# Kernel optimization log

Hardware: AMD Instinct MI355X
Metric: run time of the kernel (lower is better)

Reference implementation:

```python
import jax, jax.numpy as jnp
import numpy as np

N, E, G = 50000, 600000, 512
F_IN, H, OUT = 128, 128, 256


def setup_inputs() -> dict:
    key = jax.random.key(0)
    ks = jax.random.split(key, 16)
    x = jax.random.normal(ks[0], (N, F_IN), dtype=jnp.float32)
    edge_index = jax.random.randint(ks[1], (2, E), 0, N, dtype=jnp.int64)
    batch = jnp.sort(jax.random.randint(ks[2], (N,), 0, G, dtype=jnp.int64))
    def lin(k, out_d, in_d):
        s = 1.0 / np.sqrt(in_d)
        return jax.random.uniform(k, (out_d, in_d), jnp.float32, -s, s)
    W1l, W1r = lin(ks[3], H, F_IN), lin(ks[4], H, F_IN)
    b1 = jnp.zeros((H,), jnp.float32)
    W2l, W2r = lin(ks[5], H, H), lin(ks[6], H, H)
    b2 = jnp.zeros((H,), jnp.float32)
    W3l, W3r = lin(ks[7], H, H), lin(ks[8], H, H)
    b3 = jnp.zeros((H,), jnp.float32)
    Wlin = lin(ks[9], OUT, 2 * H)
    blin = jnp.zeros((OUT,), jnp.float32)
    return dict(x=x, edge_index=edge_index, batch=batch,
                W1l=W1l, b1=b1, W1r=W1r, W2l=W2l, b2=b2, W2r=W2r,
                W3l=W3l, b3=b3, W3r=W3r, Wlin=Wlin, blin=blin)


def reference(x, edge_index, batch, W1l, b1, W1r, W2l, b2, W2r, W3l, b3, W3r, Wlin, blin):
    src, dst = edge_index[0], edge_index[1]
    # in-degree of each target node (mean aggregation denominator)
    deg = jax.ops.segment_sum(jnp.ones((E,), x.dtype), dst, num_segments=N)
    deg = jnp.maximum(deg, 1.0)[:, None]

    def sage(h, Wl, bl, Wr):
        # mean-aggregate neighbor features then linear; plus root transform
        agg = jax.ops.segment_sum(h[src], dst, num_segments=N) / deg
        return agg @ Wl.T + bl + h @ Wr.T

    h = jax.nn.relu(sage(x, W1l, b1, W1r))
    h = jax.nn.relu(sage(h, W2l, b2, W2r))
    h = sage(h, W3l, b3, W3r)

    # global max / mean pool per graph
    x_max = jax.ops.segment_max(h, batch, num_segments=G)
    x_max = jnp.where(jnp.isfinite(x_max), x_max, 0.0)
    cnt = jnp.maximum(jax.ops.segment_sum(jnp.ones((N,), h.dtype), batch, num_segments=G), 1.0)
    x_mean = jax.ops.segment_sum(h, batch, num_segments=G) / cnt[:, None]

    pooled = jnp.concatenate([x_max, x_mean], axis=1)  # [G, 2H]
    # dropout is identity in eval mode
    return pooled @ Wlin.T + blin
```

## Files before the change

### kernel.cpp

```cpp
#include <hip/hip_runtime.h>
#include <hip/hip_bf16.h>
#include <hip/hip_fp16.h>


#define FH 128
#define OUTD 256
#define SLOTS 64
#define PWB 96

typedef unsigned int u32;
typedef unsigned short u16;
typedef __attribute__((ext_vector_type(8))) _Float16 f16frag;
typedef __attribute__((ext_vector_type(4))) float f4frag;

typedef __attribute__((address_space(3))) u32 lds_u32;
typedef __attribute__((address_space(1))) const u32 glb_u32;

__device__ inline void async_copy16(const void* g, void* l) {
    __builtin_amdgcn_global_load_lds((glb_u32*)g, (lds_u32*)l, 16, 0, 0);
}

__global__ void mega_prep(const float* __restrict__ x, u16* __restrict__ x16, int n4,
                          const float* __restrict__ W0, const float* __restrict__ W1,
                          const float* __restrict__ W2, const float* __restrict__ W3,
                          const float* __restrict__ W4, const float* __restrict__ W5,
                          uint4* __restrict__ Bf,
                          const int* __restrict__ src, const int* __restrict__ dst,
                          int* __restrict__ cursor, int* __restrict__ esrc, int E, int SC,
                          const int* __restrict__ batch, int* __restrict__ gstart,
                          int n, int g, int GBND) {
    int blk = blockIdx.x;
    if (blk < PWB) {
        int wid = blk * 4 + (threadIdx.x >> 6);
        int pair = wid >> 3;
        int ot = wid & 7;
        int ks = pair & 7;
        int arr = pair >> 3;
        int l = threadIdx.x & 63;
        const float* Ws[6] = {W0, W1, W2, W3, W4, W5};
        const float* W = Ws[arr];
        bool use_lo = (ks >= 4);
        int kb = (ks & 3) * 32 + (l >> 4) * 8;
        int o = ot * 16 + (l & 15);
        float4 v0 = *(const float4*)(W + o * 128 + kb);
        float4 v1 = *(const float4*)(W + o * 128 + kb + 4);
        float vv[8] = {v0.x, v0.y, v0.z, v0.w, v1.x, v1.y, v1.z, v1.w};
        u32 h[8];
        #pragma unroll
        for (int i = 0; i < 8; ++i) {
            float v = vv[i];
            __half hi = __float2half(v);
            if (use_lo) {
                float rem = v - __half2float(hi);
                __half lo = __float2half(rem);
                h[i] = *(u16*)&lo;
            } else {
                h[i] = *(u16*)&hi;
            }
        }
        uint4 u;
        u.x = h[0] | (h[1] << 16);
        u.y = h[2] | (h[3] << 16);
        u.z = h[4] | (h[5] << 16);
        u.w = h[6] | (h[7] << 16);
        Bf[(size_t)arr * 4096 + (ks * 8 + ot) * 64 + l] = u;
    } else if (blk < PWB + SC) {
        int e = (blk - PWB) * 256 + threadIdx.x;
        if (e < E) {
            int d = dst[e];
            int pos = atomicAdd(&cursor[d], 1);
            if (pos < SLOTS) esrc[(size_t)d * SLOTS + pos] = src[e];
        }
    } else if (blk < PWB + SC + GBND) {
        int i = (blk - PWB - SC) * 256 + threadIdx.x;
        if (i >= n) return;
        int b = batch[i];
        int pb = (i == 0) ? -1 : batch[i - 1];
        for (int q = pb + 1; q <= b; ++q) gstart[q] = i;
        if (i == n - 1) {
            for (int q = b + 1; q <= g; ++q) gstart[q] = n;
        }
    } else {
        int id = (blk - PWB - SC - GBND) * 256 + threadIdx.x;
        if (id >= n4) return;
        float4 v = *(const float4*)(x + (size_t)id * 4);
        __half h0 = __float2half(v.x), h1 = __float2half(v.y);
        __half h2 = __float2half(v.z), h3 = __float2half(v.w);
        ushort4 s;
        s.x = *(u16*)&h0; s.y = *(u16*)&h1; s.z = *(u16*)&h2; s.w = *(u16*)&h3;
        *(ushort4*)(x16 + (size_t)id * 4) = s;
    }
}

__device__ inline void add8(float* a, uint4 u) {
    float2 f0 = __half22float2(*(__half2*)&u.x);
    float2 f1 = __half22float2(*(__half2*)&u.y);
    float2 f2 = __half22float2(*(__half2*)&u.z);
    float2 f3 = __half22float2(*(__half2*)&u.w);
    a[0] += f0.x; a[1] += f0.y; a[2] += f1.x; a[3] += f1.y;
    a[4] += f2.x; a[5] += f2.y; a[6] += f3.x; a[7] += f3.y;
}

__global__ void agg_kernel(const u16* __restrict__ h16,
                           const int* __restrict__ deg, const int* __restrict__ esrc,
                           u16* __restrict__ agg16, int n_nodes) {
    int node = blockIdx.x * 16 + (threadIdx.x >> 4);
    if (node >= n_nodes) return;
    int lane = threadIdx.x & 15;
    int f = lane * 8;
    int d = deg[node];
    int s0 = node * SLOTS, s1 = s0 + min(d, SLOTS);
    float a0[8] = {0, 0, 0, 0, 0, 0, 0, 0};
    float a1[8] = {0, 0, 0, 0, 0, 0, 0, 0};
    float a2[8] = {0, 0, 0, 0, 0, 0, 0, 0};
    float a3[8] = {0, 0, 0, 0, 0, 0, 0, 0};
    int j = s0;
    for (; j + 8 <= s1; j += 8) {
        int i0 = esrc[j],     i1 = esrc[j + 1], i2 = esrc[j + 2], i3 = esrc[j + 3];
        int i4 = esrc[j + 4], i5 = esrc[j + 5], i6 = esrc[j + 6], i7 = esrc[j + 7];
        uint4 u0 = *(const uint4*)(h16 + (size_t)i0 * FH + f);
        uint4 u1 = *(const uint4*)(h16 + (size_t)i1 * FH + f);
        uint4 u2 = *(const uint4*)(h16 + (size_t)i2 * FH + f);
        uint4 u3 = *(const uint4*)(h16 + (size_t)i3 * FH + f);
        uint4 u4 = *(const uint4*)(h16 + (size_t)i4 * FH + f);
        uint4 u5 = *(const uint4*)(h16 + (size_t)i5 * FH + f);
        uint4 u6 = *(const uint4*)(h16 + (size_t)i6 * FH + f);
        uint4 u7 = *(const uint4*)(h16 + (size_t)i7 * FH + f);
        add8(a0, u0); add8(a1, u1); add8(a2, u2); add8(a3, u3);
        add8(a0, u4); add8(a1, u5); add8(a2, u6); add8(a3, u7);
    }
    if (j + 4 <= s1) {
        int i0 = esrc[j], i1 = esrc[j + 1], i2 = esrc[j + 2], i3 = esrc[j + 3];
        uint4 u0 = *(const uint4*)(h16 + (size_t)i0 * FH + f);
        uint4 u1 = *(const uint4*)(h16 + (size_t)i1 * FH + f);
        uint4 u2 = *(const uint4*)(h16 + (size_t)i2 * FH + f);
        uint4 u3 = *(const uint4*)(h16 + (size_t)i3 * FH + f);
        add8(a0, u0); add8(a1, u1); add8(a2, u2); add8(a3, u3);
        j += 4;
    }
    for (; j < s1; ++j) {
        uint4 u0 = *(const uint4*)(h16 + (size_t)esrc[j] * FH + f);
        add8(a0, u0);
    }
    float di = 1.0f / (float)max(d, 1);
    u32 oh[8];
    #pragma unroll
    for (int i = 0; i < 8; ++i) {
        __half hv = __float2half((a0[i] + a1[i] + a2[i] + a3[i]) * di);
        oh[i] = *(u16*)&hv;
    }
    uint4 w;
    w.x = oh[0] | (oh[1] << 16);
    w.y = oh[2] | (oh[3] << 16);
    w.z = oh[4] | (oh[5] << 16);
    w.w = oh[6] | (oh[7] << 16);
    *(uint4*)(agg16 + (size_t)node * FH + f) = w;
}

__global__ __launch_bounds__(256, 2)
void mfma_gemm(const u16* __restrict__ A1, const u16* __restrict__ A2,
               const uint4* __restrict__ Bf1, const uint4* __restrict__ Bf2,
               const float* __restrict__ bias, u16* __restrict__ out16,
               int do_relu) {
    __shared__ uint4 Bl[4096];
    int tid = threadIdx.x;
    int l = tid & 63;
    int wv = tid >> 6;
    int bn0 = blockIdx.x * 192 + wv * 48;
    int m = l & 15, q = l >> 4;

    f4frag acc[3][8];
    #pragma unroll
    for (int i = 0; i < 3; ++i)
        #pragma unroll
        for (int o = 0; o < 8; ++o)
            acc[i][o] = (f4frag){0.f, 0.f, 0.f, 0.f};

    #pragma unroll
    for (int p = 0; p < 2; ++p) {
        const u16* P = p ? A2 : A1;
        const uint4* Bf = p ? Bf2 : Bf1;

        f16frag Af[3][4];
        #pragma unroll
        for (int nt = 0; nt < 3; ++nt)
            #pragma unroll
            for (int s = 0; s < 4; ++s)
                Af[nt][s] = *(const f16frag*)(P + (size_t)(bn0 + nt * 16 + m) * FH + s * 32 + q * 8);

        __syncthreads();

        #pragma unroll
        for (int u = 0; u < 16; ++u)
            async_copy16(Bf + (size_t)u * 256 + wv * 64 + l,
                         &Bl[u * 256 + wv * 64]);
        __syncthreads();

        #pragma unroll
        for (int s = 0; s < 4; ++s) {
            {
                f16frag B[8];
                #pragma unroll
                for (int ot = 0; ot < 8; ++ot)
                    B[ot] = *(const f16frag*)&Bl[(size_t)(s * 8 + ot) * 64 + l];
                #pragma unroll
                for (int ot = 0; ot < 8; ++ot)
                    #pragma unroll
                    for (int nt = 0; nt < 3; ++nt)
                        acc[nt][ot] = __builtin_amdgcn_mfma_f32_16x16x32_f16(Af[nt][s], B[ot], acc[nt][ot], 0, 0, 0);
            }
            {
                f16frag B[8];
                #pragma unroll
                for (int ot = 0; ot < 8; ++ot)
                    B[ot] = *(const f16frag*)&Bl[(size_t)((s + 4) * 8 + ot) * 64 + l];
                #pragma unroll
                for (int ot = 0; ot < 8; ++ot)
                    #pragma unroll
                    for (int nt = 0; nt < 3; ++nt)
                        acc[nt][ot] = __builtin_amdgcn_mfma_f32_16x16x32_f16(Af[nt][s], B[ot], acc[nt][ot], 0, 0, 0);
            }
        }
    }

    #pragma unroll
    for (int nt = 0; nt < 3; ++nt)
        #pragma unroll
        for (int r = 0; r < 4; ++r) {
            int node = bn0 + nt * 16 + q * 4 + r;
            #pragma unroll
            for (int ot = 0; ot < 8; ++ot) {
                float v = acc[nt][ot][r] + bias[ot * 16 + m];
                if (do_relu) v = fmaxf(v, 0.f);
                __half hv = __float2half(v);
                out16[(size_t)node * FH + ot * 16 + m] = *(u16*)&hv;
            }
        }
}

__global__ __launch_bounds__(256, 2)
void pool_final(const u16* __restrict__ h16, const int* __restrict__ gstart,
                const float* __restrict__ Wlin, const float* __restrict__ blin,
                float* __restrict__ out) {
    __shared__ float smax[16][FH];
    __shared__ float ssum[16][FH];
    __shared__ float pr[2 * FH];
    int g = blockIdx.x;
    int tid = threadIdx.x;
    int way = tid >> 4;
    int lane = tid & 15;
    int f = lane * 8;
    int s = gstart[g], e = gstart[g + 1];

    float mx[8], sm[8];
    #pragma unroll
    for (int i = 0; i < 8; ++i) { mx[i] = -INFINITY; sm[i] = 0.f; }
    for (int n = s + way; n < e; n += 16) {
        uint4 u = *(const uint4*)(h16 + (size_t)n * FH + f);
        float2 f0 = __half22float2(*(__half2*)&u.x);
        float2 f1 = __half22float2(*(__half2*)&u.y);
        float2 f2 = __half22float2(*(__half2*)&u.z);
        float2 f3 = __half22float2(*(__half2*)&u.w);
        float v[8] = {f0.x, f0.y, f1.x, f1.y, f2.x, f2.y, f3.x, f3.y};
        #pragma unroll
        for (int i = 0; i < 8; ++i) {
            mx[i] = fmaxf(mx[i], v[i]);
            sm[i] += v[i];
        }
    }
    #pragma unroll
    for (int i = 0; i < 8; ++i) {
        smax[way][f + i] = mx[i];
        ssum[way][f + i] = sm[i];
    }
    __syncthreads();
    int c = e - s;
    if (tid < FH) {
        float m2 = -INFINITY, s2 = 0.f;
        #pragma unroll
        for (int w2 = 0; w2 < 16; ++w2) {
            m2 = fmaxf(m2, smax[w2][tid]);
            s2 += ssum[w2][tid];
        }
        pr[tid] = (c > 0) ? m2 : 0.f;
        pr[FH + tid] = s2 / (float)max(c, 1);
    }
    __syncthreads();
    int o = tid;
    const float4* wr = (const float4*)(Wlin + (size_t)o * (2 * FH));
    float acc = 0.f;
    #pragma unroll
    for (int j = 0; j < (2 * FH) / 4; ++j) {
        float4 wv = wr[j];
        acc += wv.x * pr[j * 4 + 0] + wv.y * pr[j * 4 + 1] +
               wv.z * pr[j * 4 + 2] + wv.w * pr[j * 4 + 3];
    }
    out[(size_t)g * OUTD + o] = acc + blin[o];
}

extern "C" void kernel_launch(void* const* d_in, const int* in_sizes, int n_in,
                              void* d_out, int out_size, void* d_ws, size_t ws_size,
                              hipStream_t stream) {
    const float* x     = (const float*)d_in[0];
    const int*   ei    = (const int*)d_in[1];
    const int*   batch = (const int*)d_in[2];
    const float* W1l = (const float*)d_in[3];
    const float* b1  = (const float*)d_in[4];
    const float* W1r = (const float*)d_in[5];
    const float* W2l = (const float*)d_in[6];
    const float* b2  = (const float*)d_in[7];
    const float* W2r = (const float*)d_in[8];
    const float* W3l = (const float*)d_in[9];
    const float* b3  = (const float*)d_in[10];
    const float* W3r = (const float*)d_in[11];
    const float* Wlin = (const float*)d_in[12];
    const float* blin = (const float*)d_in[13];
    float* out = (float*)d_out;

    const int E = in_sizes[1] / 2;
    const int N = in_sizes[2];
    const int G = out_size / OUTD;
    const int* src = ei;
    const int* dst = ei + E;
    const int GB = (N + 191) / 192;
    const int NP = GB * 192;

    char* w = (char*)d_ws;
    auto alloc = [&](size_t bytes) {
        void* p = (void*)w;
        w += (bytes + 255) & ~(size_t)255;
        return p;
    };
    int*   cursor = (int*)alloc((size_t)N * sizeof(int));
    int*   esrc   = (int*)alloc((size_t)N * SLOTS * sizeof(int));
    int*   gstart = (int*)alloc((size_t)(G + 1) * sizeof(int));
    u16*   x16    = (u16*)alloc((size_t)NP * FH * sizeof(u16));
    u16*   agg16  = (u16*)alloc((size_t)NP * FH * sizeof(u16));
    u16*   hA16   = (u16*)alloc((size_t)NP * FH * sizeof(u16));
    u16*   hB16   = (u16*)alloc((size_t)NP * FH * sizeof(u16));
    uint4* BF     = (uint4*)alloc((size_t)6 * 4096 * sizeof(uint4));
    (void)ws_size;

    hipMemsetAsync(cursor, 0, (size_t)N * sizeof(int), stream);
    const int n4 = N * 32;
    const int PX = (n4 + 255) / 256;
    const int SC = (E + 255) / 256;
    const int GBND = (N + 255) / 256;
    mega_prep<<<PWB + SC + GBND + PX, 256, 0, stream>>>(
        x, x16, n4,
        W1l, W1r, W2l, W2r, W3l, W3r, BF,
        src, dst, cursor, esrc, E, SC,
        batch, gstart, N, G, GBND);

    const int agg_grid = (N + 15) / 16;

    agg_kernel<<<agg_grid, 256, 0, stream>>>(x16, cursor, esrc, agg16, N);
    mfma_gemm<<<GB, 256, 0, stream>>>(agg16, x16, BF + 0 * 4096, BF + 1 * 4096, b1, hA16, 1);
    agg_kernel<<<agg_grid, 256, 0, stream>>>(hA16, cursor, esrc, agg16, N);
    mfma_gemm<<<GB, 256, 0, stream>>>(agg16, hA16, BF + 2 * 4096, BF + 3 * 4096, b2, hB16, 1);
    agg_kernel<<<agg_grid, 256, 0, stream>>>(hB16, cursor, esrc, agg16, N);
    mfma_gemm<<<GB, 256, 0, stream>>>(agg16, hB16, BF + 4 * 4096, BF + 5 * 4096, b3, hA16, 0);

    pool_final<<<G, 256, 0, stream>>>(hA16, gstart, Wlin, blin, out);
}
```

Before: 288.8 us.

## Split aggregation feature dimension across four blocks with 4-byte gathers

The mean-aggregation kernel now launches four blocks per 16-node chunk. Each block covers a 32-feature slice, so every lane gathers 4 bytes per neighbour instead of 16. This gives four times as many blocks for parallelism and latency hiding, at the cost of re-reading the edge index list four times and issuing many small 64-byte row-segment gathers instead of full 256-byte rows. The edge index loads are also marked nontemporal.

New measurement: 366.2 us. 26.8% more time.

```diff
diff --git a/kernel.cpp b/kernel.cpp
--- a/kernel.cpp
+++ b/kernel.cpp
@@ -92,69 +92,68 @@
     }
 }
 
-__device__ inline void add8(float* a, uint4 u) {
-    float2 f0 = __half22float2(*(__half2*)&u.x);
-    float2 f1 = __half22float2(*(__half2*)&u.y);
-    float2 f2 = __half22float2(*(__half2*)&u.z);
-    float2 f3 = __half22float2(*(__half2*)&u.w);
-    a[0] += f0.x; a[1] += f0.y; a[2] += f1.x; a[3] += f1.y;
-    a[4] += f2.x; a[5] += f2.y; a[6] += f3.x; a[7] += f3.y;
+__device__ inline void add2(float2& a, u32 w) {
+    float2 f = __half22float2(*(__half2*)&w);
+    a.x += f.x; a.y += f.y;
 }
 
 __global__ void agg_kernel(const u16* __restrict__ h16,
                            const int* __restrict__ deg, const int* __restrict__ esrc,
                            u16* __restrict__ agg16, int n_nodes) {
-    int node = blockIdx.x * 16 + (threadIdx.x >> 4);
+    int s = blockIdx.x & 3;
+    int chunk = blockIdx.x >> 2;
+    int node = chunk * 16 + (threadIdx.x >> 4);
     if (node >= n_nodes) return;
     int lane = threadIdx.x & 15;
-    int f = lane * 8;
+    int fo = s * 32 + lane * 2;
+    const u16* hp = h16 + fo;
     int d = deg[node];
     int s0 = node * SLOTS, s1 = s0 + min(d, SLOTS);
-    float a0[8] = {0, 0, 0, 0, 0, 0, 0, 0};
-    float a1[8] = {0, 0, 0, 0, 0, 0, 0, 0};
-    float a2[8] = {0, 0, 0, 0, 0, 0, 0, 0};
-    float a3[8] = {0, 0, 0, 0, 0, 0, 0, 0};
+    float2 a0 = {0.f, 0.f}, a1 = {0.f, 0.f}, a2 = {0.f, 0.f}, a3 = {0.f, 0.f};
     int j = s0;
     for (; j + 8 <= s1; j += 8) {
-        int i0 = esrc[j],     i1 = esrc[j + 1], i2 = esrc[j + 2], i3 = esrc[j + 3];
-        int i4 = esrc[j + 4], i5 = esrc[j + 5], i6 = esrc[j + 6], i7 = esrc[j + 7];
-        uint4 u0 = *(const uint4*)(h16 + (size_t)i0 * FH + f);
-        uint4 u1 = *(const uint4*)(h16 + (size_t)i1 * FH + f);
-        uint4 u2 = *(const uint4*)(h16 + (size_t)i2 * FH + f);
-        uint4 u3 = *(const uint4*)(h16 + (size_t)i3 * FH + f);
-        uint4 u4 = *(const uint4*)(h16 + (size_t)i4 * FH + f);
-        uint4 u5 = *(const uint4*)(h16 + (size_t)i5 * FH + f);
-        uint4 u6 = *(const uint4*)(h16 + (size_t)i6 * FH + f);
-        uint4 u7 = *(const uint4*)(h16 + (size_t)i7 * FH + f);
-        add8(a0, u0); add8(a1, u1); add8(a2, u2); add8(a3, u3);
-        add8(a0, u4); add8(a1, u5); add8(a2, u6); add8(a3, u7);
+        int i0 = __builtin_nontemporal_load(esrc + j);
+        int i1 = __builtin_nontemporal_load(esrc + j + 1);
+        int i2 = __builtin_nontemporal_load(esrc + j + 2);
+        int i3 = __builtin_nontemporal_load(esrc + j + 3);
+        int i4 = __builtin_nontemporal_load(esrc + j + 4);
+        int i5 = __builtin_nontemporal_load(esrc + j + 5);
+        int i6 = __builtin_nontemporal_load(esrc + j + 6);
+        int i7 = __builtin_nontemporal_load(esrc + j + 7);
+        u32 w0 = *(const u32*)(hp + (size_t)i0 * FH);
+        u32 w1 = *(const u32*)(hp + (size_t)i1 * FH);
+        u32 w2 = *(const u32*)(hp + (size_t)i2 * FH);
+        u32 w3 = *(const u32*)(hp + (size_t)i3 * FH);
+        u32 w4 = *(const u32*)(hp + (size_t)i4 * FH);
+        u32 w5 = *(const u32*)(hp + (size_t)i5 * FH);
+        u32 w6 = *(const u32*)(hp + (size_t)i6 * FH);
+        u32 w7 = *(const u32*)(hp + (size_t)i7 * FH);
+        add2(a0, w0); add2(a1, w1); add2(a2, w2); add2(a3, w3);
+        add2(a0, w4); add2(a1, w5); add2(a2, w6); add2(a3, w7);
     }
     if (j + 4 <= s1) {
-        int i0 = esrc[j], i1 = esrc[j + 1], i2 = esrc[j + 2], i3 = esrc[j + 3];
-        uint4 u0 = *(const uint4*)(h16 + (size_t)i0 * FH + f);
-        uint4 u1 = *(const uint4*)(h16 + (size_t)i1 * FH + f);
-        uint4 u2 = *(const uint4*)(h16 + (size_t)i2 * FH + f);
-        uint4 u3 = *(const uint4*)(h16 + (size_t)i3 * FH + f);
-        add8(a0, u0); add8(a1, u1); add8(a2, u2); add8(a3, u3);
+        int i0 = __builtin_nontemporal_load(esrc + j);
+        int i1 = __builtin_nontemporal_load(esrc + j + 1);
+        int i2 = __builtin_nontemporal_load(esrc + j + 2);
+        int i3 = __builtin_nontemporal_load(esrc + j + 3);
+        u32 w0 = *(const u32*)(hp + (size_t)i0 * FH);
+        u32 w1 = *(const u32*)(hp + (size_t)i1 * FH);
+        u32 w2 = *(const u32*)(hp + (size_t)i2 * FH);
+        u32 w3 = *(const u32*)(hp + (size_t)i3 * FH);
+        add2(a0, w0); add2(a1, w1); add2(a2, w2); add2(a3, w3);
         j += 4;
     }
     for (; j < s1; ++j) {
-        uint4 u0 = *(const uint4*)(h16 + (size_t)esrc[j] * FH + f);
-        add8(a0, u0);
+        int i0 = __builtin_nontemporal_load(esrc + j);
+        u32 w0 = *(const u32*)(hp + (size_t)i0 * FH);
+        add2(a0, w0);
     }
     float di = 1.0f / (float)max(d, 1);
-    u32 oh[8];
-    #pragma unroll
-    for (int i = 0; i < 8; ++i) {
-        __half hv = __float2half((a0[i] + a1[i] + a2[i] + a3[i]) * di);
-        oh[i] = *(u16*)&hv;
-    }
-    uint4 w;
-    w.x = oh[0] | (oh[1] << 16);
-    w.y = oh[2] | (oh[3] << 16);
-    w.z = oh[4] | (oh[5] << 16);
-    w.w = oh[6] | (oh[7] << 16);
-    *(uint4*)(agg16 + (size_t)node * FH + f) = w;
+    float fx = (a0.x + a1.x + a2.x + a3.x) * di;
+    float fy = (a0.y + a1.y + a2.y + a3.y) * di;
+    __half hx = __float2half(fx), hy = __float2half(fy);
+    u32 oh = (u32)(*(u16*)&hx) | ((u32)(*(u16*)&hy) << 16);
+    *(u32*)(agg16 + (size_t)node * FH + fo) = oh;
 }
 
 __global__ __launch_bounds__(256, 2)
@@ -352,7 +351,7 @@
         src, dst, cursor, esrc, E, SC,
         batch, gstart, N, G, GBND);
 
-    const int agg_grid = (N + 15) / 16;
+    const int agg_grid = ((N + 15) / 16) * 4;
 
     agg_kernel<<<agg_grid, 256, 0, stream>>>(x16, cursor, esrc, agg16, N);
     mfma_gemm<<<GB, 256, 0, stream>>>(agg16, x16, BF + 0 * 4096, BF + 1 * 4096, b1, hA16, 1);
```
